# Performance work log

Measured on AMD Instinct MI355X. Metric: run time of the kernel, lower is better.

Reference implementation:

```python
import jax, jax.numpy as jnp
import numpy as np

N = 50000
E_RAND = 800000
F_IN = 512
HID = 64
HEADS = 4
C = 40
NEG_SLOPE = 0.2  # PyG GATConv default leaky_relu slope


def setup_inputs() -> dict:
    key = jax.random.key(0)
    ks = jax.random.split(key, 12)
    x = jax.random.normal(ks[0], (N, F_IN), dtype=jnp.float32)
    # random edges + self loops (PyG GATConv add_self_loops=True)
    ei_rand = jax.random.randint(ks[1], (2, E_RAND), 0, N, dtype=jnp.int64)
    loops = jnp.broadcast_to(jnp.arange(N, dtype=jnp.int64), (2, N))
    edge_index = jnp.concatenate([ei_rand, loops], axis=1)  # [2, 850000]
    # layer 1: F_IN -> HEADS*HID, concat
    s1 = 1.0 / np.sqrt(F_IN)
    W1 = jax.random.normal(ks[2], (F_IN, HEADS * HID), dtype=jnp.float32) * s1
    a_src1 = jax.random.normal(ks[3], (HEADS, HID), dtype=jnp.float32) * (1.0 / np.sqrt(HID))
    a_dst1 = jax.random.normal(ks[4], (HEADS, HID), dtype=jnp.float32) * (1.0 / np.sqrt(HID))
    b1 = jnp.zeros((HEADS * HID,), dtype=jnp.float32)
    # layer 2: HEADS*HID -> C, 1 head, concat=False
    s2 = 1.0 / np.sqrt(HEADS * HID)
    W2 = jax.random.normal(ks[5], (HEADS * HID, C), dtype=jnp.float32) * s2
    a_src2 = jax.random.normal(ks[6], (1, C), dtype=jnp.float32) * (1.0 / np.sqrt(C))
    a_dst2 = jax.random.normal(ks[7], (1, C), dtype=jnp.float32) * (1.0 / np.sqrt(C))
    b2 = jnp.zeros((C,), dtype=jnp.float32)
    return {"x": x, "edge_index": edge_index, "W1": W1, "a_src1": a_src1,
            "a_dst1": a_dst1, "b1": b1, "W2": W2, "a_src2": a_src2,
            "a_dst2": a_dst2, "b2": b2}


def gat_conv(x, src, dst, W, a_s, a_d, b, concat):
    n = x.shape[0]
    H, D = a_s.shape
    h = (x @ W).reshape(n, H, D)                    # [N,H,D]
    al_s = jnp.einsum('nhd,hd->nh', h, a_s)          # per-node src score
    al_d = jnp.einsum('nhd,hd->nh', h, a_d)          # per-node dst score
    e = jax.nn.leaky_relu(al_s[src] + al_d[dst], NEG_SLOPE)  # [E,H]
    # segment softmax over edges grouped by destination node
    m = jax.ops.segment_max(e, dst, num_segments=n)  # [N,H]
    e = jnp.exp(e - m[dst])
    denom = jax.ops.segment_sum(e, dst, num_segments=n)
    alpha = e / (denom[dst] + 1e-16)                 # [E,H]
    msg = h[src] * alpha[:, :, None]                 # [E,H,D]
    out = jax.ops.segment_sum(msg, dst, num_segments=n)  # [N,H,D]
    out = out.reshape(n, H * D) if concat else out.mean(axis=1)
    return out + b


def reference(x, edge_index, W1, a_src1, a_dst1, b1, W2, a_src2, a_dst2, b2):
    src, dst = edge_index[0], edge_index[1]
    # dropout p=0.6 is identity in eval mode
    h = jax.nn.elu(gat_conv(x, src, dst, W1, a_src1, a_dst1, b1, concat=True))
    out = gat_conv(h, src, dst, W2, a_src2, a_dst2, b2, concat=False)
    return jax.nn.log_softmax(out, axis=1)
```

## Files before the change

### kernel.cpp

```cpp
#include <hip/hip_runtime.h>
#include <math.h>

#define NNODES 50000
#define NPAD 50176
#define FIN 512
#define HID 64
#define HEADS 4
#define HD (HEADS * HID)
#define NCLS 40
#define NCLSP 48
#define NEG_SLOPE 0.2f
#define SBLK 256
#define NSCAN ((NNODES + SBLK - 1) / SBLK)

typedef __attribute__((ext_vector_type(8))) short short8;
typedef __attribute__((ext_vector_type(4))) float f32x4;

static __device__ inline unsigned short f2bf(float f) {
    unsigned int u = __builtin_bit_cast(unsigned int, f);
    unsigned int r = (u + 0x7FFFu + ((u >> 16) & 1u)) >> 16;
    return (unsigned short)r;
}
static __device__ inline float bf2f(unsigned short b) {
    return __builtin_bit_cast(float, (unsigned int)b << 16);
}
static __device__ inline void gload_lds16(const unsigned short* g, unsigned short* l) {
    __builtin_amdgcn_global_load_lds(
        (const __attribute__((address_space(1))) unsigned int*)g,
        (__attribute__((address_space(3))) unsigned int*)l, 16, 0, 0);
}

__global__ __launch_bounds__(256) void xcast_kernel(const float* __restrict__ x,
                                                    unsigned short* __restrict__ xb) {
    const size_t idx = ((size_t)blockIdx.x * 256 + threadIdx.x) * 8;
    if (idx < (size_t)NNODES * FIN) {
        const float4 v0 = *(const float4*)&x[idx];
        const float4 v1 = *(const float4*)&x[idx + 4];
        ushort4 p0, p1;
        p0.x = f2bf(v0.x); p0.y = f2bf(v0.y); p0.z = f2bf(v0.z); p0.w = f2bf(v0.w);
        p1.x = f2bf(v1.x); p1.y = f2bf(v1.y); p1.z = f2bf(v1.z); p1.w = f2bf(v1.w);
        *(ushort4*)&xb[idx] = p0;
        *(ushort4*)&xb[idx + 4] = p1;
    } else {
        const ushort4 z = {0, 0, 0, 0};
        *(ushort4*)&xb[idx] = z;
        *(ushort4*)&xb[idx + 4] = z;
    }
}

__global__ __launch_bounds__(256) void w1t_kernel(const float* __restrict__ W1,
                                                  unsigned short* __restrict__ W1t) {
    const int idx = blockIdx.x * 256 + threadIdx.x;
    const int k = idx >> 8;
    const int n = idx & 255;
    W1t[n * FIN + k] = f2bf(W1[idx]);
}

__global__ __launch_bounds__(256) void w2t_kernel(const float* __restrict__ W2,
                                                  unsigned short* __restrict__ W2t) {
    const int idx = blockIdx.x * 256 + threadIdx.x;
    const int n = idx >> 8;
    const int k = idx & 255;
    W2t[n * HD + k] = (n < NCLS) ? f2bf(W2[k * NCLS + n]) : (unsigned short)0;
}

#define BM 64
#define BN 256
#define BK 32

__global__ __launch_bounds__(256) void gemm1_kernel(const unsigned short* __restrict__ xb,
                                                    const unsigned short* __restrict__ W1t,
                                                    const float* __restrict__ a_src,
                                                    const float* __restrict__ a_dst,
                                                    unsigned short* __restrict__ h1,
                                                    float* __restrict__ al_s,
                                                    float* __restrict__ al_d) {
    __shared__ unsigned short As[BM * BK];
    __shared__ unsigned short Bs[BN * BK];
    const int tid = threadIdx.x;
    const int wave = tid >> 6;
    const int lane = tid & 63;
    const int quad = lane >> 4;
    const int col = lane & 15;
    const int m0 = blockIdx.x * BM;
    const int srow = lane >> 2;
    const int skk = (lane & 3) * 8;

    f32x4 acc[4][4] = {};

    for (int k0 = 0; k0 < FIN; k0 += BK) {
        {
            const int r = wave * 16 + srow;
            gload_lds16(&xb[(size_t)(m0 + r) * FIN + k0 + skk], &As[r * BK + skk]);
        }
        #pragma unroll
        for (int c = 0; c < 4; ++c) {
            const int r = c * 64 + wave * 16 + srow;
            gload_lds16(&W1t[(size_t)r * FIN + k0 + skk], &Bs[r * BK + skk]);
        }
        __syncthreads();

        short8 af[4], bf[4];
        #pragma unroll
        for (int i = 0; i < 4; ++i)
            af[i] = *(const short8*)&As[(i * 16 + col) * BK + quad * 8];
        #pragma unroll
        for (int j = 0; j < 4; ++j)
            bf[j] = *(const short8*)&Bs[(wave * 64 + j * 16 + col) * BK + quad * 8];
        #pragma unroll
        for (int i = 0; i < 4; ++i)
            #pragma unroll
            for (int j = 0; j < 4; ++j)
                acc[i][j] = __builtin_amdgcn_mfma_f32_16x16x32_bf16(af[i], bf[j], acc[i][j], 0, 0, 0);
        __syncthreads();
    }

    float asv[4], adv[4];
    #pragma unroll
    for (int j = 0; j < 4; ++j) {
        asv[j] = a_src[wave * 64 + j * 16 + col];
        adv[j] = a_dst[wave * 64 + j * 16 + col];
    }
    #pragma unroll
    for (int i = 0; i < 4; ++i) {
        #pragma unroll
        for (int reg = 0; reg < 4; ++reg) {
            const int row = i * 16 + quad * 4 + reg;
            const int gm = m0 + row;
            float ds = 0.f, dd = 0.f;
            #pragma unroll
            for (int j = 0; j < 4; ++j) {
                const float v = acc[i][j][reg];
                ds = fmaf(v, asv[j], ds);
                dd = fmaf(v, adv[j], dd);
                if (gm < NNODES) {
                    const int gc = wave * 64 + j * 16 + col;
                    h1[(size_t)gm * HD + gc] = f2bf(v);
                }
            }
            #pragma unroll
            for (int off = 1; off < 16; off <<= 1) {
                ds += __shfl_xor(ds, off);
                dd += __shfl_xor(dd, off);
            }
            if (col == 0 && gm < NNODES) {
                al_s[gm * HEADS + wave] = ds;
                al_d[gm * HEADS + wave] = dd;
            }
        }
    }
}

__global__ void deg_kernel(const int* __restrict__ ei, int E, int* __restrict__ deg) {
    const int e = blockIdx.x * 256 + threadIdx.x;
    if (e < E) atomicAdd(&deg[ei[E + e]], 1);
}

__global__ __launch_bounds__(SBLK) void scan1_kernel(const int* __restrict__ deg,
                                                     int* __restrict__ psum,
                                                     int* __restrict__ bsum) {
    __shared__ int ws[4];
    const int t = threadIdx.x;
    const int idx = blockIdx.x * SBLK + t;
    const int lane = t & 63;
    const int w = t >> 6;
    int sv = (idx < NNODES) ? deg[idx] : 0;
    #pragma unroll
    for (int off = 1; off < 64; off <<= 1) {
        const int n = __shfl_up(sv, off);
        if (lane >= off) sv += n;
    }
    if (lane == 63) ws[w] = sv;
    __syncthreads();
    int add = 0;
    for (int i = 0; i < w; ++i) add += ws[i];
    sv += add;
    if (idx < NNODES) psum[idx] = sv;
    if (t == SBLK - 1) bsum[blockIdx.x] = sv;
}

__global__ __launch_bounds__(SBLK) void scan2_kernel(int* __restrict__ bsum,
                                                     int* __restrict__ offsets) {
    __shared__ int ws[4];
    const int t = threadIdx.x;
    const int lane = t & 63;
    const int w = t >> 6;
    int sv = (t < NSCAN) ? bsum[t] : 0;
    #pragma unroll
    for (int off = 1; off < 64; off <<= 1) {
        const int n = __shfl_up(sv, off);
        if (lane >= off) sv += n;
    }
    if (lane == 63) ws[w] = sv;
    __syncthreads();
    int add = 0;
    for (int i = 0; i < w; ++i) add += ws[i];
    sv += add;
    if (t < NSCAN) bsum[t] = sv;
    if (t == SBLK - 1) offsets[NNODES] = sv;
}

__global__ __launch_bounds__(SBLK) void scan3_kernel(const int* __restrict__ deg,
                                                     const int* __restrict__ psum,
                                                     const int* __restrict__ bsum,
                                                     int* __restrict__ offsets) {
    const int b = blockIdx.x;
    const int idx = b * SBLK + threadIdx.x;
    if (idx < NNODES) {
        const int boff = (b > 0) ? bsum[b - 1] : 0;
        offsets[idx] = psum[idx] - deg[idx] + boff;
    }
}

__global__ void scatter_kernel(const int* __restrict__ ei, int E,
                               const int* __restrict__ offsets,
                               int* __restrict__ cursor,
                               int* __restrict__ csr_src) {
    const int e = blockIdx.x * 256 + threadIdx.x;
    if (e < E) {
        const int dst = ei[E + e];
        const int src = ei[e];
        const int pos = offsets[dst] + atomicAdd(&cursor[dst], 1);
        csr_src[pos] = src;
    }
}

__global__ __launch_bounds__(256) void agg1_kernel(const unsigned short* __restrict__ h1,
                                                   const float* __restrict__ al_s,
                                                   const float* __restrict__ al_d,
                                                   const int* __restrict__ offsets,
                                                   const int* __restrict__ csr_src,
                                                   const float* __restrict__ b1,
                                                   unsigned short* __restrict__ h_act) {
    const int node = (blockIdx.x * 256 + threadIdx.x) >> 6;
    const int lane = threadIdx.x & 63;
    const int half = lane >> 5;
    const int fl = lane & 31;
    const int h = fl >> 3;
    const float ad = al_d[node * HEADS + h];
    const int start = offsets[node];
    const int end = offsets[node + 1];
    const int last = end - 1;

    float s = 0.f;
    float acc[8] = {};

    {
        const int idx = start + half;
        const int src = csr_src[min(idx, last)];
        float sc = (idx < end) ? al_s[src * HEADS + h] : -__builtin_inff();
        short8 v = *(const short8*)&h1[(size_t)src * HD + fl * 8];

        for (int i = start; i < end; i += 2) {
            const int j = i + 2 + half;
            const int nsrc = csr_src[min(j, last)];
            const float nsc = (j < end) ? al_s[nsrc * HEADS + h] : -__builtin_inff();
            const short8 nv = *(const short8*)&h1[(size_t)nsrc * HD + fl * 8];
            float e_ = sc + ad;
            e_ = e_ > 0.f ? e_ : NEG_SLOPE * e_;
            const float p = __expf(e_);
            s += p;
            #pragma unroll
            for (int k = 0; k < 8; ++k)
                acc[k] = fmaf(p, bf2f((unsigned short)v[k]), acc[k]);
            sc = nsc; v = nv;
        }
    }
    s += __shfl_xor(s, 32);
    #pragma unroll
    for (int k = 0; k < 8; ++k) acc[k] += __shfl_xor(acc[k], 32);

    if (half == 0) {
        const float inv = 1.f / (s + 1e-16f);
        const float4 b0 = *(const float4*)&b1[fl * 8];
        const float4 b4 = *(const float4*)&b1[fl * 8 + 4];
        float o[8];
        o[0] = acc[0] * inv + b0.x; o[1] = acc[1] * inv + b0.y;
        o[2] = acc[2] * inv + b0.z; o[3] = acc[3] * inv + b0.w;
        o[4] = acc[4] * inv + b4.x; o[5] = acc[5] * inv + b4.y;
        o[6] = acc[6] * inv + b4.z; o[7] = acc[7] * inv + b4.w;
        short8 ob;
        #pragma unroll
        for (int k = 0; k < 8; ++k) {
            const float e = o[k] > 0.f ? o[k] : expm1f(o[k]);
            ob[k] = (short)f2bf(e);
        }
        *(short8*)&h_act[(size_t)node * HD + fl * 8] = ob;
    }
}

#define G2M 64
#define BSTRIDE 264

__global__ __launch_bounds__(256) void gemm2_kernel(const unsigned short* __restrict__ h_act,
                                                    const unsigned short* __restrict__ W2t,
                                                    const float* __restrict__ a_s2,
                                                    const float* __restrict__ a_d2,
                                                    unsigned short* __restrict__ h2,
                                                    float* __restrict__ al_s,
                                                    float* __restrict__ al_d) {
    __shared__ unsigned short Bt[NCLSP][BSTRIDE];
    const int tid = threadIdx.x;
    const int wave = tid >> 6;
    const int lane = tid & 63;
    const int quad = lane >> 4;
    const int col = lane & 15;
    const int m0 = blockIdx.x * G2M;

    #pragma unroll
    for (int it = 0; it < 6; ++it) {
        const int ch = it * 256 + tid;
        const int n = ch >> 5;
        const int c8 = (ch & 31) * 8;
        *(uint4*)&Bt[n][c8] = *(const uint4*)&W2t[(size_t)n * HD + c8];
    }

    const int rowm = m0 + wave * 16 + col;
    const int arow = min(rowm, NNODES - 1);
    short8 af[8];
    #pragma unroll
    for (int ks = 0; ks < 8; ++ks)
        af[ks] = *(const short8*)&h_act[(size_t)arow * HD + ks * 32 + quad * 8];

    __syncthreads();

    f32x4 acc[3] = {};
    #pragma unroll
    for (int j = 0; j < 3; ++j) {
        #pragma unroll
        for (int ks = 0; ks < 8; ++ks) {
            const short8 bfr = *(const short8*)&Bt[j * 16 + col][ks * 32 + quad * 8];
            acc[j] = __builtin_amdgcn_mfma_f32_16x16x32_bf16(af[ks], bfr, acc[j], 0, 0, 0);
        }
    }

    float ps[4] = {0.f, 0.f, 0.f, 0.f};
    float pd[4] = {0.f, 0.f, 0.f, 0.f};
    #pragma unroll
    for (int j = 0; j < 3; ++j) {
        const int c = j * 16 + col;
        const bool cv = c < NCLS;
        const float asc = cv ? a_s2[c] : 0.f;
        const float adc = cv ? a_d2[c] : 0.f;
        #pragma unroll
        for (int reg = 0; reg < 4; ++reg) {
            const float v = acc[j][reg];
            ps[reg] += v * asc;
            pd[reg] += v * adc;
            const int node = m0 + wave * 16 + quad * 4 + reg;
            if (cv && node < NNODES)
                h2[(size_t)node * NCLS + c] = f2bf(v);
        }
    }
    #pragma unroll
    for (int reg = 0; reg < 4; ++reg) {
        #pragma unroll
        for (int off = 1; off < 16; off <<= 1) {
            ps[reg] += __shfl_xor(ps[reg], off);
            pd[reg] += __shfl_xor(pd[reg], off);
        }
    }
    if (col == 0) {
        #pragma unroll
        for (int reg = 0; reg < 4; ++reg) {
            const int node = m0 + wave * 16 + quad * 4 + reg;
            if (node < NNODES) {
                al_s[node] = ps[reg];
                al_d[node] = pd[reg];
            }
        }
    }
}

__global__ __launch_bounds__(256) void agg2_kernel(const unsigned short* __restrict__ h2,
                                                   const float* __restrict__ al_s,
                                                   const float* __restrict__ al_d,
                                                   const int* __restrict__ offsets,
                                                   const int* __restrict__ csr_src,
                                                   const float* __restrict__ b2,
                                                   float* __restrict__ out) {
    const int node = (blockIdx.x * 256 + threadIdx.x) >> 6;
    const int lane = threadIdx.x & 63;
    const int c = lane < NCLS ? lane : NCLS - 1;
    const float ad = al_d[node];
    const int start = offsets[node];
    const int end = offsets[node + 1];
    const int last = end - 1;

    float sA = 0.f, sB = 0.f, aA = 0.f, aB = 0.f;

#define PROC2(sc_, v_, s_, a_)                            \
    {                                                     \
        float e_ = sc_ + ad;                              \
        e_ = e_ > 0.f ? e_ : NEG_SLOPE * e_;              \
        const float p_ = __expf(e_);                      \
        s_ += p_;                                         \
        a_ = fmaf(p_, v_, a_);                            \
    }

    int srcA = csr_src[start];
    int srcB = csr_src[min(start + 1, last)];
    float scA = al_s[srcA];
    float scB = (start + 1 < end) ? al_s[srcB] : -__builtin_inff();
    float vA = bf2f(h2[(size_t)srcA * NCLS + c]);
    float vB = bf2f(h2[(size_t)srcB * NCLS + c]);

    for (int i = start; i < end; i += 2) {
        const int j = i + 2;
        const int nsrcA = csr_src[min(j, last)];
        const int nsrcB = csr_src[min(j + 1, last)];
        const float nscA = (j < end) ? al_s[nsrcA] : -__builtin_inff();
        const float nscB = (j + 1 < end) ? al_s[nsrcB] : -__builtin_inff();
        const float nvA = bf2f(h2[(size_t)nsrcA * NCLS + c]);
        const float nvB = bf2f(h2[(size_t)nsrcB * NCLS + c]);
        PROC2(scA, vA, sA, aA);
        PROC2(scB, vB, sB, aB);
        scA = nscA; vA = nvA; scB = nscB; vB = nvB;
    }
    const float s = sA + sB;
    const float acc = aA + aB;
#undef PROC2

    float o = acc / (s + 1e-16f) + b2[c];
    float mx = (lane < NCLS) ? o : -1e30f;
    #pragma unroll
    for (int off = 1; off < 64; off <<= 1) mx = fmaxf(mx, __shfl_xor(mx, off));
    float ex = (lane < NCLS) ? __expf(o - mx) : 0.f;
    #pragma unroll
    for (int off = 1; off < 64; off <<= 1) ex += __shfl_xor(ex, off);
    const float res = o - mx - logf(ex);
    if (lane < NCLS) out[(size_t)node * NCLS + lane] = res;
}

extern "C" void kernel_launch(void* const* d_in, const int* in_sizes, int n_in,
                              void* d_out, int out_size, void* d_ws, size_t ws_size,
                              hipStream_t stream) {
    const float* x      = (const float*)d_in[0];
    const int*   ei     = (const int*)d_in[1];
    const float* W1     = (const float*)d_in[2];
    const float* a_src1 = (const float*)d_in[3];
    const float* a_dst1 = (const float*)d_in[4];
    const float* b1     = (const float*)d_in[5];
    const float* W2     = (const float*)d_in[6];
    const float* a_src2 = (const float*)d_in[7];
    const float* a_dst2 = (const float*)d_in[8];
    const float* b2     = (const float*)d_in[9];
    float* out = (float*)d_out;
    const int E = in_sizes[1] / 2;

    char* ws = (char*)d_ws;
    size_t off = 0;
    auto alloc = [&](size_t bytes) -> char* {
        char* p = ws + off;
        off += (bytes + 255) & ~(size_t)255;
        return p;
    };
    unsigned short* xb    = (unsigned short*)alloc((size_t)NPAD * FIN * 2);
    unsigned short* W1t   = (unsigned short*)alloc((size_t)FIN * HD * 2);
    unsigned short* W2t   = (unsigned short*)alloc((size_t)NCLSP * HD * 2);
    unsigned short* h1    = (unsigned short*)alloc((size_t)NNODES * HD * 2);
    unsigned short* h_act = (unsigned short*)alloc((size_t)NNODES * HD * 2);
    unsigned short* h2    = (unsigned short*)alloc((size_t)NNODES * NCLS * 2);
    float* al_s1  = (float*)alloc((size_t)NNODES * HEADS * 4);
    float* al_d1  = (float*)alloc((size_t)NNODES * HEADS * 4);
    float* al_s2  = (float*)alloc((size_t)NNODES * 4);
    float* al_d2  = (float*)alloc((size_t)NNODES * 4);
    int*   deg    = (int*)alloc((size_t)NNODES * 4);
    int*   psum   = (int*)alloc((size_t)NNODES * 4);
    int*   bsum   = (int*)alloc((size_t)SBLK * 4);
    int*   offs   = (int*)alloc((size_t)(NNODES + 1) * 4);
    int*   cursor = (int*)alloc((size_t)NNODES * 4);
    int*   csrsrc = (int*)alloc((size_t)E * 4);

    hipMemsetAsync(deg, 0, (size_t)NNODES * 4, stream);
    hipMemsetAsync(cursor, 0, (size_t)NNODES * 4, stream);

    const int eb = (E + 255) / 256;
    xcast_kernel<<<(int)((size_t)NPAD * FIN / 8 / 256), 256, 0, stream>>>(x, xb);
    w1t_kernel<<<FIN * HD / 256, 256, 0, stream>>>(W1, W1t);
    w2t_kernel<<<NCLSP, 256, 0, stream>>>(W2, W2t);
    deg_kernel<<<eb, 256, 0, stream>>>(ei, E, deg);
    scan1_kernel<<<NSCAN, SBLK, 0, stream>>>(deg, psum, bsum);
    scan2_kernel<<<1, SBLK, 0, stream>>>(bsum, offs);
    scan3_kernel<<<NSCAN, SBLK, 0, stream>>>(deg, psum, bsum, offs);
    scatter_kernel<<<eb, 256, 0, stream>>>(ei, E, offs, cursor, csrsrc);

    gemm1_kernel<<<NPAD / BM, 256, 0, stream>>>(xb, W1t, a_src1, a_dst1, h1, al_s1, al_d1);
    agg1_kernel<<<NNODES / 4, 256, 0, stream>>>(h1, al_s1, al_d1, offs, csrsrc, b1, h_act);
    gemm2_kernel<<<(NNODES + G2M - 1) / G2M, 256, 0, stream>>>(h_act, W2t, a_src2, a_dst2, h2, al_s2, al_d2);
    agg2_kernel<<<NNODES / 4, 256, 0, stream>>>(h2, al_s2, al_d2, offs, csrsrc, b2, out);
}
```

Measured before the change: 455.9 us.

## Process more edges per wave in aggregation kernels and pad h2 to 64 classes

agg1 now processes four edges per wave concurrently, with 16 lanes each handling 16 features, where it previously processed two. agg2 moves from one lane per class to eight edges in flight, each loaded as an 8-wide bf16 vector. To make those vector loads aligned, h2 is padded to 64 columns (NCLSP=64) and gemm2 computes and stores all 64 padded columns. The aim is more memory-level parallelism in the latency-bound gather loops, at the cost of more registers, extra cross-lane reductions and a larger h2 buffer.

```diff
diff --git a/kernel.cpp b/kernel.cpp
--- a/kernel.cpp
+++ b/kernel.cpp
@@ -8,7 +8,7 @@
 #define HEADS 4
 #define HD (HEADS * HID)
 #define NCLS 40
-#define NCLSP 48
+#define NCLSP 64
 #define NEG_SLOPE 0.2f
 #define SBLK 256
 #define NSCAN ((NNODES + SBLK - 1) / SBLK)
@@ -234,58 +234,70 @@
                                                    unsigned short* __restrict__ h_act) {
     const int node = (blockIdx.x * 256 + threadIdx.x) >> 6;
     const int lane = threadIdx.x & 63;
-    const int half = lane >> 5;
-    const int fl = lane & 31;
-    const int h = fl >> 3;
+    const int q = lane >> 4;
+    const int fl = lane & 15;
+    const int h = fl >> 2;
     const float ad = al_d[node * HEADS + h];
     const int start = offsets[node];
     const int end = offsets[node + 1];
     const int last = end - 1;
 
     float s = 0.f;
-    float acc[8] = {};
+    float acc[16] = {};
 
     {
-        const int idx = start + half;
-        const int src = csr_src[min(idx, last)];
-        float sc = (idx < end) ? al_s[src * HEADS + h] : -__builtin_inff();
-        short8 v = *(const short8*)&h1[(size_t)src * HD + fl * 8];
-
-        for (int i = start; i < end; i += 2) {
-            const int j = i + 2 + half;
+        const int idx = start + q;
+        const int src0 = csr_src[min(idx, last)];
+        float sc = (idx < end) ? al_s[src0 * HEADS + h] : -__builtin_inff();
+        short8 v0 = *(const short8*)&h1[(size_t)src0 * HD + fl * 16];
+        short8 v1 = *(const short8*)&h1[(size_t)src0 * HD + fl * 16 + 8];
+
+        for (int i = start; i < end; i += 4) {
+            const int j = i + 4 + q;
             const int nsrc = csr_src[min(j, last)];
             const float nsc = (j < end) ? al_s[nsrc * HEADS + h] : -__builtin_inff();
-            const short8 nv = *(const short8*)&h1[(size_t)nsrc * HD + fl * 8];
+            const short8 nv0 = *(const short8*)&h1[(size_t)nsrc * HD + fl * 16];
+            const short8 nv1 = *(const short8*)&h1[(size_t)nsrc * HD + fl * 16 + 8];
             float e_ = sc + ad;
             e_ = e_ > 0.f ? e_ : NEG_SLOPE * e_;
             const float p = __expf(e_);
             s += p;
             #pragma unroll
             for (int k = 0; k < 8; ++k)
-                acc[k] = fmaf(p, bf2f((unsigned short)v[k]), acc[k]);
-            sc = nsc; v = nv;
-        }
-    }
+                acc[k] = fmaf(p, bf2f((unsigned short)v0[k]), acc[k]);
+            #pragma unroll
+            for (int k = 0; k < 8; ++k)
+                acc[8 + k] = fmaf(p, bf2f((unsigned short)v1[k]), acc[8 + k]);
+            sc = nsc; v0 = nv0; v1 = nv1;
+        }
+    }
+    s += __shfl_xor(s, 16);
     s += __shfl_xor(s, 32);
     #pragma unroll
-    for (int k = 0; k < 8; ++k) acc[k] += __shfl_xor(acc[k], 32);
-
-    if (half == 0) {
+    for (int k = 0; k < 16; ++k) {
+        acc[k] += __shfl_xor(acc[k], 16);
+        acc[k] += __shfl_xor(acc[k], 32);
+    }
+
+    if (q == 0) {
         const float inv = 1.f / (s + 1e-16f);
-        const float4 b0 = *(const float4*)&b1[fl * 8];
-        const float4 b4 = *(const float4*)&b1[fl * 8 + 4];
-        float o[8];
-        o[0] = acc[0] * inv + b0.x; o[1] = acc[1] * inv + b0.y;
-        o[2] = acc[2] * inv + b0.z; o[3] = acc[3] * inv + b0.w;
-        o[4] = acc[4] * inv + b4.x; o[5] = acc[5] * inv + b4.y;
-        o[6] = acc[6] * inv + b4.z; o[7] = acc[7] * inv + b4.w;
-        short8 ob;
+        float bb[16];
+        *(float4*)&bb[0]  = *(const float4*)&b1[fl * 16];
+        *(float4*)&bb[4]  = *(const float4*)&b1[fl * 16 + 4];
+        *(float4*)&bb[8]  = *(const float4*)&b1[fl * 16 + 8];
+        *(float4*)&bb[12] = *(const float4*)&b1[fl * 16 + 12];
+        short8 ob0, ob1;
         #pragma unroll
         for (int k = 0; k < 8; ++k) {
-            const float e = o[k] > 0.f ? o[k] : expm1f(o[k]);
-            ob[k] = (short)f2bf(e);
-        }
-        *(short8*)&h_act[(size_t)node * HD + fl * 8] = ob;
+            const float o0 = acc[k] * inv + bb[k];
+            const float o1 = acc[8 + k] * inv + bb[8 + k];
+            const float e0 = o0 > 0.f ? o0 : expm1f(o0);
+            const float e1 = o1 > 0.f ? o1 : expm1f(o1);
+            ob0[k] = (short)f2bf(e0);
+            ob1[k] = (short)f2bf(e1);
+        }
+        *(short8*)&h_act[(size_t)node * HD + fl * 16] = ob0;
+        *(short8*)&h_act[(size_t)node * HD + fl * 16 + 8] = ob1;
     }
 }
 
@@ -308,7 +320,7 @@
     const int m0 = blockIdx.x * G2M;
 
     #pragma unroll
-    for (int it = 0; it < 6; ++it) {
+    for (int it = 0; it < 8; ++it) {
         const int ch = it * 256 + tid;
         const int n = ch >> 5;
         const int c8 = (ch & 31) * 8;
@@ -324,9 +336,9 @@
 
     __syncthreads();
 
-    f32x4 acc[3] = {};
-    #pragma unroll
-    for (int j = 0; j < 3; ++j) {
+    f32x4 acc[4] = {};
+    #pragma unroll
+    for (int j = 0; j < 4; ++j) {
         #pragma unroll
         for (int ks = 0; ks < 8; ++ks) {
             const short8 bfr = *(const short8*)&Bt[j * 16 + col][ks * 32 + quad * 8];
@@ -337,7 +349,7 @@
     float ps[4] = {0.f, 0.f, 0.f, 0.f};
     float pd[4] = {0.f, 0.f, 0.f, 0.f};
     #pragma unroll
-    for (int j = 0; j < 3; ++j) {
+    for (int j = 0; j < 4; ++j) {
         const int c = j * 16 + col;
         const bool cv = c < NCLS;
         const float asc = cv ? a_s2[c] : 0.f;
@@ -348,8 +360,8 @@
             ps[reg] += v * asc;
             pd[reg] += v * adc;
             const int node = m0 + wave * 16 + quad * 4 + reg;
-            if (cv && node < NNODES)
-                h2[(size_t)node * NCLS + c] = f2bf(v);
+            if (node < NNODES)
+                h2[(size_t)node * NCLSP + c] = f2bf(v);
         }
     }
     #pragma unroll
@@ -381,55 +393,77 @@
                                                    float* __restrict__ out) {
     const int node = (blockIdx.x * 256 + threadIdx.x) >> 6;
     const int lane = threadIdx.x & 63;
-    const int c = lane < NCLS ? lane : NCLS - 1;
+    const int oct = lane >> 3;
+    const int fl = lane & 7;
     const float ad = al_d[node];
     const int start = offsets[node];
     const int end = offsets[node + 1];
     const int last = end - 1;
 
-    float sA = 0.f, sB = 0.f, aA = 0.f, aB = 0.f;
-
-#define PROC2(sc_, v_, s_, a_)                            \
-    {                                                     \
-        float e_ = sc_ + ad;                              \
-        e_ = e_ > 0.f ? e_ : NEG_SLOPE * e_;              \
-        const float p_ = __expf(e_);                      \
-        s_ += p_;                                         \
-        a_ = fmaf(p_, v_, a_);                            \
-    }
-
-    int srcA = csr_src[start];
-    int srcB = csr_src[min(start + 1, last)];
-    float scA = al_s[srcA];
-    float scB = (start + 1 < end) ? al_s[srcB] : -__builtin_inff();
-    float vA = bf2f(h2[(size_t)srcA * NCLS + c]);
-    float vB = bf2f(h2[(size_t)srcB * NCLS + c]);
-
-    for (int i = start; i < end; i += 2) {
-        const int j = i + 2;
-        const int nsrcA = csr_src[min(j, last)];
-        const int nsrcB = csr_src[min(j + 1, last)];
-        const float nscA = (j < end) ? al_s[nsrcA] : -__builtin_inff();
-        const float nscB = (j + 1 < end) ? al_s[nsrcB] : -__builtin_inff();
-        const float nvA = bf2f(h2[(size_t)nsrcA * NCLS + c]);
-        const float nvB = bf2f(h2[(size_t)nsrcB * NCLS + c]);
-        PROC2(scA, vA, sA, aA);
-        PROC2(scB, vB, sB, aB);
-        scA = nscA; vA = nvA; scB = nscB; vB = nvB;
-    }
-    const float s = sA + sB;
-    const float acc = aA + aB;
-#undef PROC2
-
-    float o = acc / (s + 1e-16f) + b2[c];
-    float mx = (lane < NCLS) ? o : -1e30f;
-    #pragma unroll
-    for (int off = 1; off < 64; off <<= 1) mx = fmaxf(mx, __shfl_xor(mx, off));
-    float ex = (lane < NCLS) ? __expf(o - mx) : 0.f;
-    #pragma unroll
-    for (int off = 1; off < 64; off <<= 1) ex += __shfl_xor(ex, off);
-    const float res = o - mx - logf(ex);
-    if (lane < NCLS) out[(size_t)node * NCLS + lane] = res;
+    float s = 0.f;
+    float acc[8] = {};
+
+    {
+        const int idx = start + oct;
+        const int src0 = csr_src[min(idx, last)];
+        float sc = (idx < end) ? al_s[src0] : -__builtin_inff();
+        short8 v = *(const short8*)&h2[(size_t)src0 * NCLSP + fl * 8];
+
+        for (int i = start; i < end; i += 8) {
+            const int j = i + 8 + oct;
+            const int nsrc = csr_src[min(j, last)];
+            const float nsc = (j < end) ? al_s[nsrc] : -__builtin_inff();
+            const short8 nv = *(const short8*)&h2[(size_t)nsrc * NCLSP + fl * 8];
+            float e_ = sc + ad;
+            e_ = e_ > 0.f ? e_ : NEG_SLOPE * e_;
+            const float p = __expf(e_);
+            s += p;
+            #pragma unroll
+            for (int k = 0; k < 8; ++k)
+                acc[k] = fmaf(p, bf2f((unsigned short)v[k]), acc[k]);
+            sc = nsc; v = nv;
+        }
+    }
+    s += __shfl_xor(s, 8);
+    s += __shfl_xor(s, 16);
+    s += __shfl_xor(s, 32);
+    #pragma unroll
+    for (int k = 0; k < 8; ++k) {
+        acc[k] += __shfl_xor(acc[k], 8);
+        acc[k] += __shfl_xor(acc[k], 16);
+        acc[k] += __shfl_xor(acc[k], 32);
+    }
+
+    if (oct == 0) {
+        const float inv = 1.f / (s + 1e-16f);
+        float o[8];
+        float mx = -1e30f;
+        #pragma unroll
+        for (int k = 0; k < 8; ++k) {
+            const int c = fl * 8 + k;
+            const float bc = (c < NCLS) ? b2[c] : 0.f;
+            o[k] = acc[k] * inv + bc;
+            if (c < NCLS) mx = fmaxf(mx, o[k]);
+        }
+        #pragma unroll
+        for (int off = 1; off < 8; off <<= 1) mx = fmaxf(mx, __shfl_xor(mx, off));
+        float ex = 0.f;
+        #pragma unroll
+        for (int k = 0; k < 8; ++k) {
+            const int c = fl * 8 + k;
+            if (c < NCLS) ex += __expf(o[k] - mx);
+        }
+        #pragma unroll
+        for (int off = 1; off < 8; off <<= 1) ex += __shfl_xor(ex, off);
+        const float lse = mx + logf(ex);
+        if (fl < 5) {
+            float4 r0, r1;
+            r0.x = o[0] - lse; r0.y = o[1] - lse; r0.z = o[2] - lse; r0.w = o[3] - lse;
+            r1.x = o[4] - lse; r1.y = o[5] - lse; r1.z = o[6] - lse; r1.w = o[7] - lse;
+            *(float4*)&out[(size_t)node * NCLS + fl * 8] = r0;
+            *(float4*)&out[(size_t)node * NCLS + fl * 8 + 4] = r1;
+        }
+    }
 }
 
 extern "C" void kernel_launch(void* const* d_in, const int* in_sizes, int n_in,
@@ -460,7 +494,7 @@
     unsigned short* W2t   = (unsigned short*)alloc((size_t)NCLSP * HD * 2);
     unsigned short* h1    = (unsigned short*)alloc((size_t)NNODES * HD * 2);
     unsigned short* h_act = (unsigned short*)alloc((size_t)NNODES * HD * 2);
-    unsigned short* h2    = (unsigned short*)alloc((size_t)NNODES * NCLS * 2);
+    unsigned short* h2    = (unsigned short*)alloc((size_t)NNODES * NCLSP * 2);
     float* al_s1  = (float*)alloc((size_t)NNODES * HEADS * 4);
     float* al_d1  = (float*)alloc((size_t)NNODES * HEADS * 4);
     float* al_s2  = (float*)alloc((size_t)NNODES * 4);
```

Result: faster. 427.6 us (-6.2%).
